# Kernel tuning notes

Measured on AMD Instinct MI355X. Metric: run time of the kernel, lower is better.

The kernel has to match this reference:

```python
import jax, jax.numpy as jnp
import numpy as np

B, L, D, H = 4, 2048, 1024, 16
HD = D // H

def setup_inputs() -> dict:
    key = jax.random.key(0)
    k1, k2, k3, k4 = jax.random.split(key, 4)
    return {
        "Q": jax.random.normal(k1, (B, L, D), dtype=jnp.float32),
        "K": jax.random.normal(k2, (B, L, D), dtype=jnp.float32),
        "V": jax.random.normal(k3, (B, L, D), dtype=jnp.float32),
        "W_out": jax.random.normal(k4, (D, D), dtype=jnp.float32) * (1.0 / np.sqrt(D)),
        "b_out": jnp.zeros((D,), dtype=jnp.float32),
    }

def reference(Q, K, V, W_out, b_out):
    b, l, d = Q.shape
    h, hd = H, d // H
    q = Q.reshape(b, l, h, hd)
    k = K.reshape(b, l, h, hd)
    v = V.reshape(b, l, h, hd)
    # energy: [b, h, q, k]
    energy = jnp.einsum('nqhd,nkhd->nhqk', q, k)
    # NOTE: original scales by sqrt(embed_dim), not sqrt(head_dim)
    attn = jax.nn.softmax(energy / jnp.sqrt(jnp.float32(d)), axis=-1)
    out = jnp.einsum('nhql,nlhd->nqhd', attn, v).reshape(b, l, d)
    # torch nn.Linear: x @ W.T + b
    return out @ W_out.T + b_out
```

## Files before the change

### kernel.cpp

```cpp
#include <hip/hip_runtime.h>
#include <hip/hip_bf16.h>


#define B_  4
#define L_  2048
#define D_  1024
#define H_  16

typedef float  f32x4  __attribute__((ext_vector_type(4)));
typedef float  f32x16 __attribute__((ext_vector_type(16)));
typedef short  bf16x8 __attribute__((ext_vector_type(8)));
typedef short  bf16x4 __attribute__((ext_vector_type(4)));

__device__ inline unsigned short f2bf(float x) {
    union { float f; unsigned u; } v; v.f = x;
    unsigned r = v.u + 0x7FFFu + ((v.u >> 16) & 1u);
    return (unsigned short)(r >> 16);
}
__device__ inline float fast_exp2(float x) {
#if __has_builtin(__builtin_amdgcn_exp2f)
    return __builtin_amdgcn_exp2f(x);
#else
    return exp2f(x);
#endif
}
__device__ inline bf16x8 pack8s(float4 a, float4 b, float s) {
    bf16x8 r;
    r[0] = (short)f2bf(a.x * s); r[1] = (short)f2bf(a.y * s);
    r[2] = (short)f2bf(a.z * s); r[3] = (short)f2bf(a.w * s);
    r[4] = (short)f2bf(b.x * s); r[5] = (short)f2bf(b.y * s);
    r[6] = (short)f2bf(b.z * s); r[7] = (short)f2bf(b.w * s);
    return r;
}
__device__ inline unsigned cvtpk(float lo, float hi) {
    unsigned r;
    asm("v_cvt_pk_bf16_f32 %0, %1, %2" : "=v"(r) : "v"(lo), "v"(hi));
    return r;
}
#define PSWAP(a, b) asm("v_permlane32_swap_b32 %0, %1" : "+v"(a), "+v"(b))

__device__ inline f32x16 zero16() {
    f32x16 z;
    #pragma unroll
    for (int i = 0; i < 16; ++i) z[i] = 0.f;
    return z;
}
__device__ inline void gld16(const void* g, void* l) {
    __builtin_amdgcn_global_load_lds(
        (const __attribute__((address_space(1))) void*)g,
        (__attribute__((address_space(3))) void*)l, 16, 0, 0);
}

__global__ __launch_bounds__(256) void convw_kernel(const float* __restrict__ W,
                                                    unsigned short* __restrict__ Wb) {
    int i = (blockIdx.x * 256 + threadIdx.x) * 4;
    float4 v = *(const float4*)&W[i];
    bf16x4 o;
    o[0] = (short)f2bf(v.x); o[1] = (short)f2bf(v.y);
    o[2] = (short)f2bf(v.z); o[3] = (short)f2bf(v.w);
    *(bf16x4*)&Wb[i] = o;
}

__global__ __launch_bounds__(256) void convk_kernel(const float* __restrict__ K,
                                                    unsigned short* __restrict__ Kb) {
    int o = blockIdx.x * 256 + threadIdx.x;
    int d8 = o & 7; int h = (o >> 3) & 15; int key = (o >> 7) & 2047; int b = o >> 18;
    size_t base = ((size_t)(b * L_ + key) * H_ + h) * 64;
    const float* p = K + base + d8 * 8;
    float4 a = *(const float4*)p, c = *(const float4*)(p + 4);
    bf16x8 r;
    r[0] = (short)f2bf(a.x); r[1] = (short)f2bf(a.y); r[2] = (short)f2bf(a.z); r[3] = (short)f2bf(a.w);
    r[4] = (short)f2bf(c.x); r[5] = (short)f2bf(c.y); r[6] = (short)f2bf(c.z); r[7] = (short)f2bf(c.w);
    *(bf16x8*)&Kb[base + ((d8 * 8) ^ ((key & 7) * 8))] = r;
}

__global__ __launch_bounds__(256) void convv_kernel(const float* __restrict__ V,
                                                    unsigned short* __restrict__ Vb) {
    __shared__ __align__(16) unsigned short T[64 * 72];
    int tid = threadIdx.x;
    int kb_ = blockIdx.x & 31, bh = blockIdx.x >> 5;
    int b = bh >> 4, h = bh & 15, k0 = kb_ * 64;
    int kl = tid >> 4;
    int d4 = (tid & 15) * 4;
    #pragma unroll
    for (int pp = 0; pp < 4; ++pp) {
        int key = pp * 16 + kl;
        const float* p = V + ((size_t)(b * L_ + k0 + key)) * D_ + h * 64 + d4;
        float4 v = *(const float4*)p;
        T[(d4 + 0) * 72 + key] = f2bf(v.x);
        T[(d4 + 1) * 72 + key] = f2bf(v.y);
        T[(d4 + 2) * 72 + key] = f2bf(v.z);
        T[(d4 + 3) * 72 + key] = f2bf(v.w);
    }
    __syncthreads();
    #pragma unroll
    for (int i = 0; i < 2; ++i) {
        int c = i * 256 + tid; int d = c >> 3, ch = c & 7;
        bf16x8 v = *(const bf16x8*)&T[d * 72 + ch * 8];
        *(bf16x8*)&Vb[((size_t)(b * H_ + h) * 64 + d) * L_ + k0 + ((ch ^ (d & 7)) * 8)] = v;
    }
}

__global__ __launch_bounds__(256, 4) void attn_kernel(const float* __restrict__ Qg,
                                                      const unsigned short* __restrict__ Kb,
                                                      const unsigned short* __restrict__ Vb,
                                                      unsigned short* __restrict__ Og) {
    __shared__ __align__(16) unsigned short Ks[2][64 * 64];
    __shared__ __align__(16) unsigned short Vt[2][64 * 64];

    const int tid  = threadIdx.x;
    const int w    = tid >> 6;
    const int lane = tid & 63;
    const int l31  = lane & 31;
    const int hl   = lane >> 5;
    const int r7   = l31 & 7;

    const int x   = blockIdx.x;
    const int idx = x >> 3;
    const int bh  = (x & 7) * 8 + (idx & 7);
    const int qb  = idx >> 3;
    const int bz  = bh >> 4;
    const int h   = bh & 15;
    const int q0  = qb * 128;

    const float qscale = 0.04508422f;
    bf16x8 bq[4];
    {
        const int qrow = q0 + w * 32 + l31;
        const float* qp = Qg + ((size_t)(bz * L_ + qrow)) * D_ + h * 64 + hl * 8;
        #pragma unroll
        for (int dstep = 0; dstep < 4; ++dstep)
            bq[dstep] = pack8s(*(const float4*)(qp + dstep * 16),
                               *(const float4*)(qp + dstep * 16 + 4), qscale);
    }

    f32x16 o[2];
    o[0] = zero16(); o[1] = zero16();
    float lsum = 0.f;

    const unsigned short* Kbh = Kb + ((size_t)bz * L_ * H_ + h) * 64;
    const unsigned short* Vbh = Vb + (size_t)(bz * H_ + h) * 64 * L_;

    #define ISSUE(T, BUF)                                                           \
        {                                                                           \
            int k0_ = (T) * 64;                                                     \
            _Pragma("unroll")                                                       \
            for (int i = 0; i < 2; ++i) {                                           \
                int c = i * 256 + tid; int rr = c >> 3, jj = c & 7;                 \
                gld16(Kbh + (size_t)(k0_ + rr) * (H_ * 64) + jj * 8,                \
                      (char*)Ks[BUF] + (i * 256 + w * 64) * 16);                    \
                gld16(Vbh + (size_t)rr * L_ + k0_ + jj * 8,                         \
                      (char*)Vt[BUF] + (i * 256 + w * 64) * 16);                    \
            }                                                                       \
        }

    ISSUE(0, 0)

    for (int t = 0; t < 32; ++t) {
        __syncthreads();
        if (t < 31) ISSUE(t + 1, (t + 1) & 1)
        const unsigned short* ks = Ks[t & 1];
        const unsigned short* vt = Vt[t & 1];

        #pragma unroll
        for (int kk = 0; kk < 2; ++kk) {
            f32x16 s = zero16();
            #pragma unroll
            for (int dstep = 0; dstep < 4; ++dstep) {
                bf16x8 kf = *(const bf16x8*)&ks[(kk * 32 + l31) * 64 +
                                                ((((dstep << 1) | hl) ^ r7) << 3)];
                s = __builtin_amdgcn_mfma_f32_32x32x16_bf16(kf, bq[dstep], s, 0, 0, 0);
            }

            float p_[16];
            #pragma unroll
            for (int r = 0; r < 16; ++r) p_[r] = fast_exp2(s[r]);
            lsum += ((p_[0] + p_[1]) + (p_[2] + p_[3])) + ((p_[4] + p_[5]) + (p_[6] + p_[7]))
                  + ((p_[8] + p_[9]) + (p_[10] + p_[11])) + ((p_[12] + p_[13]) + (p_[14] + p_[15]));
            unsigned pk_[8];
            #pragma unroll
            for (int j = 0; j < 8; ++j) pk_[j] = cvtpk(p_[2 * j], p_[2 * j + 1]);
            PSWAP(pk_[0], pk_[2]); PSWAP(pk_[1], pk_[3]);
            PSWAP(pk_[4], pk_[6]); PSWAP(pk_[5], pk_[7]);
            union { unsigned u[4]; bf16x8 v; } a0_, a1_;
            a0_.u[0] = pk_[0]; a0_.u[1] = pk_[1]; a0_.u[2] = pk_[2]; a0_.u[3] = pk_[3];
            a1_.u[0] = pk_[4]; a1_.u[1] = pk_[5]; a1_.u[2] = pk_[6]; a1_.u[3] = pk_[7];

            #pragma unroll
            for (int kh = 0; kh < 2; ++kh) {
                const bf16x8 pf = kh ? a1_.v : a0_.v;
                const int kk2 = kk * 2 + kh;
                bf16x8 v0 = *(const bf16x8*)&vt[(l31) * 64 +
                                                ((((kk2 << 1) | hl) ^ r7) << 3)];
                bf16x8 v1 = *(const bf16x8*)&vt[(32 + l31) * 64 +
                                                ((((kk2 << 1) | hl) ^ r7) << 3)];
                o[0] = __builtin_amdgcn_mfma_f32_32x32x16_bf16(pf, v0, o[0], 0, 0, 0);
                o[1] = __builtin_amdgcn_mfma_f32_32x32x16_bf16(pf, v1, o[1], 0, 0, 0);
            }
        }
    }

    float tot = lsum + __shfl_xor(lsum, 32);
    float inv = 1.0f / tot;
    const size_t rowb0 = ((size_t)(bz * L_ + q0 + w * 32)) * D_ + h * 64;
    #pragma unroll
    for (int r = 0; r < 16; ++r) {
        const int qloc = (r & 3) + 8 * (r >> 2) + 4 * hl;
        const float invr = __shfl(inv, qloc);
        unsigned short* op = Og + rowb0 + (size_t)qloc * D_;
        op[l31]      = f2bf(o[0][r] * invr);
        op[32 + l31] = f2bf(o[1][r] * invr);
    }
}

__global__ __launch_bounds__(256, 2) void proj_kernel(const unsigned short* __restrict__ Og,
                                                      const unsigned short* __restrict__ Wb,
                                                      const float* __restrict__ bias,
                                                      float* __restrict__ Yg) {
    __shared__ unsigned short As[2][128 * 64];
    __shared__ unsigned short Bs[2][128 * 64];

    const int tid  = threadIdx.x;
    const int w    = tid >> 6;
    const int lane = tid & 63;
    const int l16  = lane & 15;
    const int quad = lane >> 4;
    const int wm   = w & 1, wn = w >> 1;

    const int m0 = blockIdx.x * 128;
    const int n0 = blockIdx.y * 128;

    f32x4 acc[4][4];
    #pragma unroll
    for (int i = 0; i < 4; ++i)
        #pragma unroll
        for (int j = 0; j < 4; ++j) acc[i][j] = (f32x4){0.f, 0.f, 0.f, 0.f};

    #define PISSUE(T, BUF)                                                          \
        {                                                                           \
            int kt_ = (T) * 64;                                                     \
            _Pragma("unroll")                                                       \
            for (int i = 0; i < 4; ++i) {                                           \
                int c = i * 256 + tid; int row = c >> 3, p = c & 7;                 \
                int j = p ^ (row & 7);                                              \
                gld16(&Og[(size_t)(m0 + row) * 1024 + kt_ + j * 8],                 \
                      (char*)As[BUF] + (i * 256 + w * 64) * 16);                    \
                gld16(&Wb[(size_t)(n0 + row) * 1024 + kt_ + j * 8],                 \
                      (char*)Bs[BUF] + (i * 256 + w * 64) * 16);                    \
            }                                                                       \
        }

    PISSUE(0, 0)

    for (int t = 0; t < 16; ++t) {
        __syncthreads();
        if (t < 15) PISSUE(t + 1, (t + 1) & 1)
        const unsigned short* as = As[t & 1];
        const unsigned short* bs = Bs[t & 1];

        #pragma unroll
        for (int ksq = 0; ksq < 2; ++ksq) {
            bf16x8 a[4], b[4];
            #pragma unroll
            for (int mt = 0; mt < 4; ++mt) {
                int row = wm * 64 + mt * 16 + l16;
                a[mt] = *(const bf16x8*)&as[row * 64 + (((ksq * 4 + quad) ^ (l16 & 7)) * 8)];
            }
            #pragma unroll
            for (int nt = 0; nt < 4; ++nt) {
                int row = wn * 64 + nt * 16 + l16;
                b[nt] = *(const bf16x8*)&bs[row * 64 + (((ksq * 4 + quad) ^ (l16 & 7)) * 8)];
            }
            #pragma unroll
            for (int mt = 0; mt < 4; ++mt)
                #pragma unroll
                for (int nt = 0; nt < 4; ++nt)
                    acc[mt][nt] = __builtin_amdgcn_mfma_f32_16x16x32_bf16(a[mt], b[nt], acc[mt][nt], 0, 0, 0);
        }
    }

    #pragma unroll
    for (int mt = 0; mt < 4; ++mt)
        #pragma unroll
        for (int nt = 0; nt < 4; ++nt) {
            int e = n0 + wn * 64 + nt * 16 + l16;
            float bv = bias[e];
            #pragma unroll
            for (int r = 0; r < 4; ++r) {
                int m = m0 + wm * 64 + mt * 16 + quad * 4 + r;
                Yg[(size_t)m * 1024 + e] = acc[mt][nt][r] + bv;
            }
        }
}

extern "C" void kernel_launch(void* const* d_in, const int* in_sizes, int n_in,
                              void* d_out, int out_size, void* d_ws, size_t ws_size,
                              hipStream_t stream) {
    const float* Q    = (const float*)d_in[0];
    const float* K    = (const float*)d_in[1];
    const float* V    = (const float*)d_in[2];
    const float* W    = (const float*)d_in[3];
    const float* bias = (const float*)d_in[4];
    float* Y = (float*)d_out;

    unsigned short* Og = (unsigned short*)d_ws;
    unsigned short* Wb = (unsigned short*)((char*)d_ws + (size_t)16 * 1024 * 1024);
    unsigned short* Kb = (unsigned short*)d_out;
    unsigned short* Vb = Kb + (size_t)B_ * H_ * L_ * 64;

    convw_kernel<<<D_ * D_ / (256 * 4), 256, 0, stream>>>(W, Wb);
    convk_kernel<<<B_ * L_ * H_ * 8 / 256, 256, 0, stream>>>(K, Kb);
    convv_kernel<<<B_ * H_ * (L_ / 64), 256, 0, stream>>>(V, Vb);
    attn_kernel<<<B_ * H_ * (L_ / 128), 256, 0, stream>>>(Q, Kb, Vb, Og);
    dim3 pg(B_ * L_ / 128, D_ / 128);
    proj_kernel<<<pg, 256, 0, stream>>>(Og, Wb, bias, Y);
}
```

Measured before the change: 237.6 us.

## Fuse conversion kernels, triple-buffer attention K/V loads, and swizzle projection grid

Merges the three fp32-to-bf16 conversion kernels into one launch that picks its role by block index, which removes two kernel launches. The attention kernel goes from double to triple buffering in shared memory and uses explicit vmcnt waits with raw barriers, so loads for two tiles ahead stay in flight while the current tile is computed. The projection kernel uses a 1D grid with a grouped block-to-tile mapping meant to improve L2 reuse. The extra LDS buffer raises shared memory per block, which may limit occupancy under launch_bounds(256,4).

```diff
diff --git a/kernel.cpp b/kernel.cpp
--- a/kernel.cpp
+++ b/kernel.cpp
@@ -51,53 +51,56 @@
         (__attribute__((address_space(3))) void*)l, 16, 0, 0);
 }
 
-__global__ __launch_bounds__(256) void convw_kernel(const float* __restrict__ W,
-                                                    unsigned short* __restrict__ Wb) {
-    int i = (blockIdx.x * 256 + threadIdx.x) * 4;
-    float4 v = *(const float4*)&W[i];
-    bf16x4 o;
-    o[0] = (short)f2bf(v.x); o[1] = (short)f2bf(v.y);
-    o[2] = (short)f2bf(v.z); o[3] = (short)f2bf(v.w);
-    *(bf16x4*)&Wb[i] = o;
-}
-
-__global__ __launch_bounds__(256) void convk_kernel(const float* __restrict__ K,
-                                                    unsigned short* __restrict__ Kb) {
-    int o = blockIdx.x * 256 + threadIdx.x;
-    int d8 = o & 7; int h = (o >> 3) & 15; int key = (o >> 7) & 2047; int b = o >> 18;
-    size_t base = ((size_t)(b * L_ + key) * H_ + h) * 64;
-    const float* p = K + base + d8 * 8;
-    float4 a = *(const float4*)p, c = *(const float4*)(p + 4);
-    bf16x8 r;
-    r[0] = (short)f2bf(a.x); r[1] = (short)f2bf(a.y); r[2] = (short)f2bf(a.z); r[3] = (short)f2bf(a.w);
-    r[4] = (short)f2bf(c.x); r[5] = (short)f2bf(c.y); r[6] = (short)f2bf(c.z); r[7] = (short)f2bf(c.w);
-    *(bf16x8*)&Kb[base + ((d8 * 8) ^ ((key & 7) * 8))] = r;
-}
-
-__global__ __launch_bounds__(256) void convv_kernel(const float* __restrict__ V,
-                                                    unsigned short* __restrict__ Vb) {
+__global__ __launch_bounds__(256) void conv_fused(const float* __restrict__ W,
+                                                  unsigned short* __restrict__ Wb,
+                                                  const float* __restrict__ K,
+                                                  unsigned short* __restrict__ Kb,
+                                                  const float* __restrict__ V,
+                                                  unsigned short* __restrict__ Vb) {
     __shared__ __align__(16) unsigned short T[64 * 72];
-    int tid = threadIdx.x;
-    int kb_ = blockIdx.x & 31, bh = blockIdx.x >> 5;
-    int b = bh >> 4, h = bh & 15, k0 = kb_ * 64;
-    int kl = tid >> 4;
-    int d4 = (tid & 15) * 4;
-    #pragma unroll
-    for (int pp = 0; pp < 4; ++pp) {
-        int key = pp * 16 + kl;
-        const float* p = V + ((size_t)(b * L_ + k0 + key)) * D_ + h * 64 + d4;
-        float4 v = *(const float4*)p;
-        T[(d4 + 0) * 72 + key] = f2bf(v.x);
-        T[(d4 + 1) * 72 + key] = f2bf(v.y);
-        T[(d4 + 2) * 72 + key] = f2bf(v.z);
-        T[(d4 + 3) * 72 + key] = f2bf(v.w);
-    }
-    __syncthreads();
-    #pragma unroll
-    for (int i = 0; i < 2; ++i) {
-        int c = i * 256 + tid; int d = c >> 3, ch = c & 7;
-        bf16x8 v = *(const bf16x8*)&T[d * 72 + ch * 8];
-        *(bf16x8*)&Vb[((size_t)(b * H_ + h) * 64 + d) * L_ + k0 + ((ch ^ (d & 7)) * 8)] = v;
+    const int bid = blockIdx.x;
+    const int tid = threadIdx.x;
+
+    if (bid < 1024) {
+        int i = (bid * 256 + tid) * 4;
+        float4 v = *(const float4*)&W[i];
+        bf16x4 o;
+        o[0] = (short)f2bf(v.x); o[1] = (short)f2bf(v.y);
+        o[2] = (short)f2bf(v.z); o[3] = (short)f2bf(v.w);
+        *(bf16x4*)&Wb[i] = o;
+    } else if (bid < 5120) {
+        int o = (bid - 1024) * 256 + tid;
+        int d8 = o & 7; int h = (o >> 3) & 15; int key = (o >> 7) & 2047; int b = o >> 18;
+        size_t base = ((size_t)(b * L_ + key) * H_ + h) * 64;
+        const float* p = K + base + d8 * 8;
+        float4 a = *(const float4*)p, c = *(const float4*)(p + 4);
+        bf16x8 r;
+        r[0] = (short)f2bf(a.x); r[1] = (short)f2bf(a.y); r[2] = (short)f2bf(a.z); r[3] = (short)f2bf(a.w);
+        r[4] = (short)f2bf(c.x); r[5] = (short)f2bf(c.y); r[6] = (short)f2bf(c.z); r[7] = (short)f2bf(c.w);
+        *(bf16x8*)&Kb[base + ((d8 * 8) ^ ((key & 7) * 8))] = r;
+    } else {
+        int vb_ = bid - 5120;
+        int kb_ = vb_ & 31, bh = vb_ >> 5;
+        int b = bh >> 4, h = bh & 15, k0 = kb_ * 64;
+        int kl = tid >> 4;
+        int d4 = (tid & 15) * 4;
+        #pragma unroll
+        for (int pp = 0; pp < 4; ++pp) {
+            int key = pp * 16 + kl;
+            const float* p = V + ((size_t)(b * L_ + k0 + key)) * D_ + h * 64 + d4;
+            float4 v = *(const float4*)p;
+            T[(d4 + 0) * 72 + key] = f2bf(v.x);
+            T[(d4 + 1) * 72 + key] = f2bf(v.y);
+            T[(d4 + 2) * 72 + key] = f2bf(v.z);
+            T[(d4 + 3) * 72 + key] = f2bf(v.w);
+        }
+        __syncthreads();
+        #pragma unroll
+        for (int i = 0; i < 2; ++i) {
+            int c = i * 256 + tid; int d = c >> 3, ch = c & 7;
+            bf16x8 v = *(const bf16x8*)&T[d * 72 + ch * 8];
+            *(bf16x8*)&Vb[((size_t)(b * H_ + h) * 64 + d) * L_ + k0 + ((ch ^ (d & 7)) * 8)] = v;
+        }
     }
 }
 
@@ -105,8 +108,8 @@
                                                       const unsigned short* __restrict__ Kb,
                                                       const unsigned short* __restrict__ Vb,
                                                       unsigned short* __restrict__ Og) {
-    __shared__ __align__(16) unsigned short Ks[2][64 * 64];
-    __shared__ __align__(16) unsigned short Vt[2][64 * 64];
+    __shared__ __align__(16) unsigned short Ks[3][64 * 64];
+    __shared__ __align__(16) unsigned short Vt[3][64 * 64];
 
     const int tid  = threadIdx.x;
     const int w    = tid >> 6;
@@ -154,51 +157,64 @@
             }                                                                       \
         }
 
+    #define COMP(KSP, VTP)                                                          \
+        {                                                                           \
+            const unsigned short* ks = (KSP);                                       \
+            const unsigned short* vt = (VTP);                                       \
+            _Pragma("unroll")                                                       \
+            for (int kk = 0; kk < 2; ++kk) {                                        \
+                f32x16 s = zero16();                                                \
+                _Pragma("unroll")                                                   \
+                for (int dstep = 0; dstep < 4; ++dstep) {                           \
+                    bf16x8 kf = *(const bf16x8*)&ks[(kk * 32 + l31) * 64 +          \
+                                                    ((((dstep << 1) | hl) ^ r7) << 3)]; \
+                    s = __builtin_amdgcn_mfma_f32_32x32x16_bf16(kf, bq[dstep], s, 0, 0, 0); \
+                }                                                                   \
+                float p_[16];                                                       \
+                _Pragma("unroll")                                                   \
+                for (int r = 0; r < 16; ++r) p_[r] = fast_exp2(s[r]);               \
+                lsum += ((p_[0] + p_[1]) + (p_[2] + p_[3])) + ((p_[4] + p_[5]) + (p_[6] + p_[7])) \
+                      + ((p_[8] + p_[9]) + (p_[10] + p_[11])) + ((p_[12] + p_[13]) + (p_[14] + p_[15])); \
+                unsigned pk_[8];                                                    \
+                _Pragma("unroll")                                                   \
+                for (int j = 0; j < 8; ++j) pk_[j] = cvtpk(p_[2 * j], p_[2 * j + 1]); \
+                PSWAP(pk_[0], pk_[2]); PSWAP(pk_[1], pk_[3]);                       \
+                PSWAP(pk_[4], pk_[6]); PSWAP(pk_[5], pk_[7]);                       \
+                union { unsigned u[4]; bf16x8 v; } a0_, a1_;                        \
+                a0_.u[0] = pk_[0]; a0_.u[1] = pk_[1]; a0_.u[2] = pk_[2]; a0_.u[3] = pk_[3]; \
+                a1_.u[0] = pk_[4]; a1_.u[1] = pk_[5]; a1_.u[2] = pk_[6]; a1_.u[3] = pk_[7]; \
+                _Pragma("unroll")                                                   \
+                for (int kh = 0; kh < 2; ++kh) {                                    \
+                    const bf16x8 pf = kh ? a1_.v : a0_.v;                           \
+                    const int kk2 = kk * 2 + kh;                                    \
+                    bf16x8 v0 = *(const bf16x8*)&vt[(l31) * 64 +                    \
+                                                    ((((kk2 << 1) | hl) ^ r7) << 3)]; \
+                    bf16x8 v1 = *(const bf16x8*)&vt[(32 + l31) * 64 +               \
+                                                    ((((kk2 << 1) | hl) ^ r7) << 3)]; \
+                    o[0] = __builtin_amdgcn_mfma_f32_32x32x16_bf16(pf, v0, o[0], 0, 0, 0); \
+                    o[1] = __builtin_amdgcn_mfma_f32_32x32x16_bf16(pf, v1, o[1], 0, 0, 0); \
+                }                                                                   \
+            }                                                                       \
+        }
+
     ISSUE(0, 0)
-
-    for (int t = 0; t < 32; ++t) {
-        __syncthreads();
-        if (t < 31) ISSUE(t + 1, (t + 1) & 1)
-        const unsigned short* ks = Ks[t & 1];
-        const unsigned short* vt = Vt[t & 1];
-
-        #pragma unroll
-        for (int kk = 0; kk < 2; ++kk) {
-            f32x16 s = zero16();
-            #pragma unroll
-            for (int dstep = 0; dstep < 4; ++dstep) {
-                bf16x8 kf = *(const bf16x8*)&ks[(kk * 32 + l31) * 64 +
-                                                ((((dstep << 1) | hl) ^ r7) << 3)];
-                s = __builtin_amdgcn_mfma_f32_32x32x16_bf16(kf, bq[dstep], s, 0, 0, 0);
-            }
-
-            float p_[16];
-            #pragma unroll
-            for (int r = 0; r < 16; ++r) p_[r] = fast_exp2(s[r]);
-            lsum += ((p_[0] + p_[1]) + (p_[2] + p_[3])) + ((p_[4] + p_[5]) + (p_[6] + p_[7]))
-                  + ((p_[8] + p_[9]) + (p_[10] + p_[11])) + ((p_[12] + p_[13]) + (p_[14] + p_[15]));
-            unsigned pk_[8];
-            #pragma unroll
-            for (int j = 0; j < 8; ++j) pk_[j] = cvtpk(p_[2 * j], p_[2 * j + 1]);
-            PSWAP(pk_[0], pk_[2]); PSWAP(pk_[1], pk_[3]);
-            PSWAP(pk_[4], pk_[6]); PSWAP(pk_[5], pk_[7]);
-            union { unsigned u[4]; bf16x8 v; } a0_, a1_;
-            a0_.u[0] = pk_[0]; a0_.u[1] = pk_[1]; a0_.u[2] = pk_[2]; a0_.u[3] = pk_[3];
-            a1_.u[0] = pk_[4]; a1_.u[1] = pk_[5]; a1_.u[2] = pk_[6]; a1_.u[3] = pk_[7];
-
-            #pragma unroll
-            for (int kh = 0; kh < 2; ++kh) {
-                const bf16x8 pf = kh ? a1_.v : a0_.v;
-                const int kk2 = kk * 2 + kh;
-                bf16x8 v0 = *(const bf16x8*)&vt[(l31) * 64 +
-                                                ((((kk2 << 1) | hl) ^ r7) << 3)];
-                bf16x8 v1 = *(const bf16x8*)&vt[(32 + l31) * 64 +
-                                                ((((kk2 << 1) | hl) ^ r7) << 3)];
-                o[0] = __builtin_amdgcn_mfma_f32_32x32x16_bf16(pf, v0, o[0], 0, 0, 0);
-                o[1] = __builtin_amdgcn_mfma_f32_32x32x16_bf16(pf, v1, o[1], 0, 0, 0);
-            }
-        }
-    }
+    ISSUE(1, 1)
+
+    #pragma unroll 3
+    for (int t = 0; t < 30; ++t) {
+        asm volatile("s_waitcnt vmcnt(4)" ::: "memory");
+        __builtin_amdgcn_s_barrier();
+        const int b2 = (t + 2) % 3;
+        ISSUE(t + 2, b2)
+        const int bt = t % 3;
+        COMP(Ks[bt], Vt[bt])
+    }
+    asm volatile("s_waitcnt vmcnt(4)" ::: "memory");
+    __builtin_amdgcn_s_barrier();
+    COMP(Ks[0], Vt[0])
+    asm volatile("s_waitcnt vmcnt(0)" ::: "memory");
+    __builtin_amdgcn_s_barrier();
+    COMP(Ks[1], Vt[1])
 
     float tot = lsum + __shfl_xor(lsum, 32);
     float inv = 1.0f / tot;
@@ -227,8 +243,12 @@
     const int quad = lane >> 4;
     const int wm   = w & 1, wn = w >> 1;
 
-    const int m0 = blockIdx.x * 128;
-    const int n0 = blockIdx.y * 128;
+    const int bid = blockIdx.x;
+    const int jj_ = bid >> 3;
+    const int mb  = (bid & 7) + 8 * (jj_ >> 3);
+    const int nb  = jj_ & 7;
+    const int m0 = mb * 128;
+    const int n0 = nb * 128;
 
     f32x4 acc[4][4];
     #pragma unroll
@@ -308,10 +328,7 @@
     unsigned short* Kb = (unsigned short*)d_out;
     unsigned short* Vb = Kb + (size_t)B_ * H_ * L_ * 64;
 
-    convw_kernel<<<D_ * D_ / (256 * 4), 256, 0, stream>>>(W, Wb);
-    convk_kernel<<<B_ * L_ * H_ * 8 / 256, 256, 0, stream>>>(K, Kb);
-    convv_kernel<<<B_ * H_ * (L_ / 64), 256, 0, stream>>>(V, Vb);
+    conv_fused<<<1024 + 4096 + 2048, 256, 0, stream>>>(W, Wb, K, Kb, V, Vb);
     attn_kernel<<<B_ * H_ * (L_ / 128), 256, 0, stream>>>(Q, Kb, Vb, Og);
-    dim3 pg(B_ * L_ / 128, D_ / 128);
-    proj_kernel<<<pg, 256, 0, stream>>>(Og, Wb, bias, Y);
-}
+    proj_kernel<<<B_ * L_ / 128 * (D_ / 128), 256, 0, stream>>>(Og, Wb, bias, Y);
+}
```

Result: slower. 243.4 us (+2.4%).
